# Kernel tuning notes

Hardware: AMD Instinct MI355X
Metric: run time of the kernel (lower is better)

Reference implementation:

```python
import jax, jax.numpy as jnp
import numpy as np

N, C, T, V = 16, 64, 512, 25
R, O, S = 8, 64, 3  # rel_channels, out_channels, num_subset


def setup_inputs() -> dict:
    key = jax.random.key(0)
    ks = jax.random.split(key, 12)
    sc = 0.05
    return {
        "x": jax.random.normal(ks[0], (N, C, T, V), jnp.float32),
        "A": jax.random.normal(ks[1], (S, V, V), jnp.float32) * 0.1,
        "alpha": jax.random.normal(ks[2], (1,), jnp.float32) * 0.1,
        "w1": jax.random.normal(ks[3], (S, R, C), jnp.float32) * sc,
        "b1": jax.random.normal(ks[4], (S, R), jnp.float32) * sc,
        "w2": jax.random.normal(ks[5], (S, R, C), jnp.float32) * sc,
        "b2": jax.random.normal(ks[6], (S, R), jnp.float32) * sc,
        "w3": jax.random.normal(ks[7], (S, O, C), jnp.float32) * sc,
        "b3": jax.random.normal(ks[8], (S, O), jnp.float32) * sc,
        "w4": jax.random.normal(ks[9], (S, O, R), jnp.float32) * sc,
        "b4": jax.random.normal(ks[10], (S, O), jnp.float32) * sc,
        "sparse": 0,
    }


def _mask(w, thr):
    # SparseConv2d: magnitude-threshold the 1x1 conv weights at runtime.
    return jnp.where(jnp.abs(w) > thr, w, jnp.zeros_like(w))


def reference(x, A, alpha, w1, b1, w2, b2, w3, b3, w4, b4, sparse):
    thr = jnp.float32(sparse)

    def conv1x1(w, b, inp):  # w [o,c], b [o], inp [n,c,t,v] -> [n,o,t,v]
        return jnp.einsum('oc,nctv->notv', _mask(w, thr), inp) + b[None, :, None, None]

    y = None
    for i in range(A.shape[0]):
        x1 = conv1x1(w1[i], b1[i], x).mean(-2)          # [n,r,v]
        x2 = conv1x1(w2[i], b2[i], x).mean(-2)          # [n,r,v]
        x3 = conv1x1(w3[i], b3[i], x)                   # [n,o,t,v]
        att = jnp.tanh(x1[..., :, None] - x2[..., None, :])  # [n,r,v,v]
        a = jnp.einsum('or,nruv->nouv', _mask(w4[i], thr), att) + b4[i][None, :, None, None]
        a = a * alpha + A[i][None, None]                # [n,o,v,v]
        z = jnp.einsum('ncuv,nctu->nctv', a, x3)        # node aggregation
        y = z if y is None else y + z
    # in_channels == out_channels -> residual is identity
    return jax.nn.relu(y + x)
```

## Files before the change

kernel.cpp:

```cpp
#include <hip/hip_runtime.h>
#include <cmath>

typedef __bf16 bf16x4v __attribute__((ext_vector_type(4)));
typedef __bf16 bf16x8 __attribute__((ext_vector_type(8)));
typedef float f32x4 __attribute__((ext_vector_type(4)));

namespace {
constexpr int kN = 16, kC = 64, kT = 512, kV = 25, kS = 3, kO = 64;
constexpr int kTV = kT * kV;
constexpr size_t WS_AFRAG = 102400;
constexpr size_t WS_W3F = WS_AFRAG + (size_t)48 * 131072;
constexpr size_t WS_XBF = WS_W3F + 3 * 8192;
}

__device__ __forceinline__ int swzB16(int c, int t, int ubyte) {
  return (c << 10) + (((t << 6) + ubyte) ^ ((((c ^ t) & 7)) << 4));
}

__global__ __launch_bounds__(256) void k1_cvt(const float* __restrict__ x,
                                              __bf16* __restrict__ xbf,
                                              float* __restrict__ xm) {
  const int bid = blockIdx.x;
  __shared__ float part[250][4];
  const int tid = threadIdx.x;
  const float4* xg4 = (const float4*)(x + (size_t)bid * kTV);
  bf16x4v* xb4 = (bf16x4v*)(xbf + (size_t)bid * kTV);
  if (tid < 250) {
    float a0 = 0.f, a1 = 0.f, a2 = 0.f, a3 = 0.f;
    for (int j = tid; j < 3200; j += 250) {
      float4 v = xg4[j];
      a0 += v.x; a1 += v.y; a2 += v.z; a3 += v.w;
      bf16x4v o;
      o[0] = (__bf16)v.x; o[1] = (__bf16)v.y;
      o[2] = (__bf16)v.z; o[3] = (__bf16)v.w;
      xb4[j] = o;
    }
    part[tid][0] = a0; part[tid][1] = a1; part[tid][2] = a2; part[tid][3] = a3;
  }
  __syncthreads();
  if (tid < 25) {
    float s = 0.f;
#pragma unroll
    for (int r = 0; r < 4; ++r) {
      int q = ((tid - r + 25) % 25) * 19 % 25;
#pragma unroll
      for (int p = 0; p < 10; ++p) s += part[q + 25 * p][r];
    }
    xm[bid * 25 + tid] = s * (1.f / 512.f);
  }
}

__global__ __launch_bounds__(256) void k2_attn(
    const float* __restrict__ xm, const float* __restrict__ Ag,
    const float* __restrict__ alpha, const float* __restrict__ w1,
    const float* __restrict__ b1, const float* __restrict__ w2,
    const float* __restrict__ b2, const float* __restrict__ w3,
    const float* __restrict__ w4, const float* __restrict__ b4,
    const int* __restrict__ sparse, unsigned char* __restrict__ ws) {
  const float thr = (float)sparse[0];
  const int b = blockIdx.x;
  const int s = b >> 6, n = (b >> 2) & 15, q = b & 3;
  __shared__ float xm_l[1600];
  __shared__ float x1_l[200], x2_l[200];
  __shared__ float att_l[8 * 625];
  __shared__ float attsum_l[200];
  __shared__ float ag_l[625];
  __shared__ float acs_l[25];
  __shared__ float w4_l[512];
  const int tid = threadIdx.x;
  for (int i = tid; i < 1600; i += 256) xm_l[i] = xm[n * 1600 + i];
  for (int i = tid; i < 512; i += 256) {
    float w = w4[s * 512 + i];
    w4_l[i] = (fabsf(w) > thr) ? w : 0.f;
  }
  for (int i = tid; i < 625; i += 256) ag_l[i] = Ag[s * 625 + i];
  __syncthreads();
  for (int i = tid; i < 400; i += 256) {
    int which = i / 200, idx = i % 200, r = idx / 25, u = idx % 25;
    const float* wrow = (which == 0 ? w1 : w2) + (s * 8 + r) * 64;
    float acc = 0.f;
    for (int cc = 0; cc < 64; ++cc) {
      float w = wrow[cc];
      w = (fabsf(w) > thr) ? w : 0.f;
      acc += w * xm_l[cc * 25 + u];
    }
    acc += (which == 0 ? b1 : b2)[s * 8 + r];
    if (which == 0) x1_l[idx] = acc;
    else x2_l[idx] = acc;
  }
  __syncthreads();
  for (int i = tid; i < 8 * 625; i += 256) {
    int r = i / 625, uv = i % 625, u = uv / 25, v = uv % 25;
    att_l[i] = tanhf(x1_l[r * 25 + u] - x2_l[r * 25 + v]);
  }
  __syncthreads();
  if (tid < 200) {
    int r = tid / 25, v = tid % 25;
    float sum = 0.f;
    for (int u = 0; u < 25; ++u) sum += att_l[r * 625 + u * 25 + v];
    attsum_l[tid] = sum;
  } else if (tid < 225) {
    int v = tid - 200;
    float sum = 0.f;
    for (int u = 0; u < 25; ++u) sum += ag_l[u * 25 + v];
    acs_l[v] = sum;
  }
  __syncthreads();
  const float al = alpha[0];
  unsigned char* afrag = ws + WS_AFRAG + (size_t)(s * 16 + n) * 131072;
  for (int slot = q * 2048 + tid; slot < (q + 1) * 2048; slot += 256) {
    int c = slot >> 7, vt = (slot >> 6) & 1, l = slot & 63;
    int v = vt * 16 + (l & 15), g = l >> 4;
    bf16x8 out;
    if (v < 25) {
      float b4v = b4[s * 64 + c];
#pragma unroll
      for (int j = 0; j < 8; ++j) {
        int u = g * 8 + j;
        float val = 0.f;
        if (u < 25) {
          float acc = 0.f;
#pragma unroll
          for (int r = 0; r < 8; ++r) acc += w4_l[c * 8 + r] * att_l[r * 625 + u * 25 + v];
          val = al * (acc + b4v) + ag_l[u * 25 + v];
        } else if (u == 25) {
          float acc = 0.f;
#pragma unroll
          for (int r = 0; r < 8; ++r) acc += w4_l[c * 8 + r] * attsum_l[r * 25 + v];
          val = al * acc + 25.f * al * b4v + acs_l[v];
        }
        out[j] = (__bf16)val;
      }
    } else {
#pragma unroll
      for (int j = 0; j < 8; ++j) out[j] = (__bf16)0.f;
    }
    *(bf16x8*)(afrag + (size_t)slot * 16) = out;
  }
  if (n == 0 && tid < 128) {
    unsigned char* w3f = ws + WS_W3F + (size_t)s * 8192;
    int slot = q * 128 + tid;
    int ot = slot >> 7, ks = (slot >> 6) & 1, l = slot & 63;
    int o = ot * 16 + (l & 15), g = l >> 4;
    bf16x8 out;
#pragma unroll
    for (int j = 0; j < 8; ++j) {
      int cp = ks * 32 + g * 8 + j;
      float w = w3[(s * 64 + o) * 64 + cp];
      out[j] = (__bf16)((fabsf(w) > thr) ? w : 0.f);
    }
    *(bf16x8*)(w3f + slot * 16) = out;
  }
}

__global__ __launch_bounds__(512) void k3_main(const __bf16* __restrict__ xbf,
                                               const float* __restrict__ b3,
                                               const unsigned char* __restrict__ ws,
                                               float* __restrict__ y) {
  const int n = blockIdx.x;
  const int tb = blockIdx.y;
  extern __shared__ __align__(16) unsigned char smem[];
  const int tid = threadIdx.x;
  const int w = tid >> 6, l = tid & 63, g = l >> 4, l15 = l & 15;

  for (int idx = tid; idx < 3072; idx += 512) {
    int pair = idx / 3, k = idx % 3;
    int c = pair >> 4, t = pair & 15;
    *(unsigned int*)(smem + swzB16(c, t, 52 + 4 * k)) = 0u;
  }

  bf16x8 xa[4][2];
#pragma unroll
  for (int cti = 0; cti < 4; ++cti)
#pragma unroll
    for (int kf = 0; kf < 2; ++kf)
#pragma unroll
      for (int j = 0; j < 8; ++j) xa[cti][kf][j] = (__bf16)0.f;
  {
    const __bf16* xbp = xbf + (size_t)n * kC * kTV;
#pragma unroll
    for (int cti = 0; cti < 4; ++cti) {
      int tt = tb * 16 + 2 * w + (cti >> 1);
      int u = (cti & 1) * 16 + l15;
      if (u < 25) {
#pragma unroll
        for (int kf = 0; kf < 2; ++kf)
#pragma unroll
          for (int j = 0; j < 8; ++j) {
            int cp = kf * 32 + g * 8 + j;
            xa[cti][kf][j] = xbp[(size_t)cp * kTV + tt * 25 + u];
          }
      }
    }
  }

  const unsigned char* afrag = ws + WS_AFRAG;
  const unsigned char* w3f = ws + WS_W3F;

  f32x4 zacc[8][2];
#pragma unroll
  for (int cc = 0; cc < 8; ++cc)
#pragma unroll
    for (int vt = 0; vt < 2; ++vt) {
      f32x4 zz = {0.f, 0.f, 0.f, 0.f};
      zacc[cc][vt] = zz;
    }

  for (int s = 0; s < kS; ++s) {
    bf16x8 B2[8][2];
    const unsigned char* af = afrag + (size_t)(s * 16 + n) * 131072;
#pragma unroll
    for (int cc = 0; cc < 8; ++cc) {
      int c = w * 8 + cc;
#pragma unroll
      for (int vt = 0; vt < 2; ++vt)
        B2[cc][vt] = *(const bf16x8*)(af + ((c * 2 + vt) * 64 + l) * 16);
    }
    ((f32x4*)(smem + 65536))[tid] =
        ((const f32x4*)(w3f + (size_t)s * 8192))[tid];
    __syncthreads();

    const unsigned char* w3l = smem + 65536;
#pragma unroll
    for (int ot = 0; ot < 4; ++ot) {
      bf16x8 wk0 = *(const bf16x8*)(w3l + ((ot * 2 + 0) * 64 + l) * 16);
      bf16x8 wk1 = *(const bf16x8*)(w3l + ((ot * 2 + 1) * 64 + l) * 16);
      int c = ot * 16 + l15;
#pragma unroll
      for (int cti = 0; cti < 4; ++cti) {
        f32x4 d = {0.f, 0.f, 0.f, 0.f};
        d = __builtin_amdgcn_mfma_f32_16x16x32_bf16(xa[cti][0], wk0, d, 0, 0, 0);
        d = __builtin_amdgcn_mfma_f32_16x16x32_bf16(xa[cti][1], wk1, d, 0, 0, 0);
        int tt = 2 * w + (cti >> 1);
        if (!(cti & 1)) {
          bf16x4v pk;
          pk[0] = (__bf16)d[0]; pk[1] = (__bf16)d[1];
          pk[2] = (__bf16)d[2]; pk[3] = (__bf16)d[3];
          *(bf16x4v*)(smem + swzB16(c, tt, g * 8)) = pk;
        } else if (g < 2) {
          bf16x4v pk;
          pk[0] = (__bf16)d[0]; pk[1] = (__bf16)d[1];
          pk[2] = (__bf16)d[2]; pk[3] = (__bf16)d[3];
          *(bf16x4v*)(smem + swzB16(c, tt, 32 + g * 8)) = pk;
        } else if (g == 2) {
          *(__bf16*)(smem + swzB16(c, tt, 48)) = (__bf16)d[0];
        }
      }
    }
    for (int i = tid; i < 1024; i += 512) {
      int c = i >> 4, t = i & 15;
      *(__bf16*)(smem + swzB16(c, t, 50)) = (__bf16)b3[s * 64 + c];
    }
    __syncthreads();
#pragma unroll
    for (int cc = 0; cc < 8; ++cc) {
      int c = w * 8 + cc;
      bf16x8 a2 = *(const bf16x8*)(smem + swzB16(c, l15, g * 16));
      zacc[cc][0] = __builtin_amdgcn_mfma_f32_16x16x32_bf16(a2, B2[cc][0], zacc[cc][0], 0, 0, 0);
      zacc[cc][1] = __builtin_amdgcn_mfma_f32_16x16x32_bf16(a2, B2[cc][1], zacc[cc][1], 0, 0, 0);
    }
  }
  __syncthreads();
  float* zs = (float*)smem;
  const __bf16* xbp = xbf + (size_t)n * kC * kTV;
  float4* yg4 = (float4*)(y + (size_t)n * kC * kTV);
#pragma unroll
  for (int h = 0; h < 2; ++h) {
    if ((w >> 2) == h) {
      int c0l = (w & 3) * 8;
#pragma unroll
      for (int cc = 0; cc < 8; ++cc)
#pragma unroll
        for (int vt = 0; vt < 2; ++vt) {
          int v = vt * 16 + l15;
          if (v < 25) {
#pragma unroll
            for (int jj = 0; jj < 4; ++jj)
              zs[(c0l + cc) * 400 + (g * 4 + jj) * 25 + v] = zacc[cc][vt][jj];
          }
        }
    }
    __syncthreads();
    for (int i4 = tid; i4 < 3200; i4 += 512) {
      int cl = i4 / 100, r4 = i4 % 100, c = h * 32 + cl;
      bf16x4v xv = *(const bf16x4v*)(xbp + (size_t)c * kTV + tb * 400 + r4 * 4);
      f32x4 zv = *(const f32x4*)(zs + cl * 400 + r4 * 4);
      float4 o;
      o.x = fmaxf(zv[0] + (float)xv[0], 0.f);
      o.y = fmaxf(zv[1] + (float)xv[1], 0.f);
      o.z = fmaxf(zv[2] + (float)xv[2], 0.f);
      o.w = fmaxf(zv[3] + (float)xv[3], 0.f);
      yg4[c * 3200 + tb * 100 + r4] = o;
    }
    __syncthreads();
  }
}

extern "C" void kernel_launch(void* const* d_in, const int* in_sizes, int n_in,
                              void* d_out, int out_size, void* d_ws, size_t ws_size,
                              hipStream_t stream) {
  const float* x = (const float*)d_in[0];
  const float* Ag = (const float*)d_in[1];
  const float* alpha = (const float*)d_in[2];
  const float* w1 = (const float*)d_in[3];
  const float* b1 = (const float*)d_in[4];
  const float* w2 = (const float*)d_in[5];
  const float* b2 = (const float*)d_in[6];
  const float* w3 = (const float*)d_in[7];
  const float* b3 = (const float*)d_in[8];
  const float* w4 = (const float*)d_in[9];
  const float* b4 = (const float*)d_in[10];
  const int* sparse = (const int*)d_in[11];

  unsigned char* ws = (unsigned char*)d_ws;
  float* xm = (float*)ws;
  __bf16* xbf = (__bf16*)(ws + WS_XBF);
  float* y = (float*)d_out;

  hipFuncSetAttribute((const void*)k3_main,
                      hipFuncAttributeMaxDynamicSharedMemorySize, 73728);

  k1_cvt<<<kN * kC, 256, 0, stream>>>(x, xbf, xm);
  k2_attn<<<kS * kN * 4, 256, 0, stream>>>(xm, Ag, alpha, w1, b1, w2, b2, w3, w4,
                                           b4, sparse, ws);
  dim3 g3(kN, kT / 16);
  k3_main<<<g3, 512, 73728, stream>>>(xbf, b3, ws, y);
}
```

Before: 74.49 us.

## Fuse three kernels into one cooperative kernel with grid-wide syncs

```diff
diff --git a/kernel.cpp b/kernel.cpp
--- a/kernel.cpp
+++ b/kernel.cpp
@@ -1,5 +1,8 @@
 #include <hip/hip_runtime.h>
+#include <hip/hip_cooperative_groups.h>
 #include <cmath>
+
+namespace cg = cooperative_groups;
 
 typedef __bf16 bf16x4v __attribute__((ext_vector_type(4)));
 typedef __bf16 bf16x8 __attribute__((ext_vector_type(8)));
@@ -17,167 +20,180 @@
   return (c << 10) + (((t << 6) + ubyte) ^ ((((c ^ t) & 7)) << 4));
 }
 
-__global__ __launch_bounds__(256) void k1_cvt(const float* __restrict__ x,
-                                              __bf16* __restrict__ xbf,
-                                              float* __restrict__ xm) {
-  const int bid = blockIdx.x;
-  __shared__ float part[250][4];
-  const int tid = threadIdx.x;
-  const float4* xg4 = (const float4*)(x + (size_t)bid * kTV);
-  bf16x4v* xb4 = (bf16x4v*)(xbf + (size_t)bid * kTV);
-  if (tid < 250) {
-    float a0 = 0.f, a1 = 0.f, a2 = 0.f, a3 = 0.f;
-    for (int j = tid; j < 3200; j += 250) {
-      float4 v = xg4[j];
-      a0 += v.x; a1 += v.y; a2 += v.z; a3 += v.w;
-      bf16x4v o;
-      o[0] = (__bf16)v.x; o[1] = (__bf16)v.y;
-      o[2] = (__bf16)v.z; o[3] = (__bf16)v.w;
-      xb4[j] = o;
-    }
-    part[tid][0] = a0; part[tid][1] = a1; part[tid][2] = a2; part[tid][3] = a3;
-  }
-  __syncthreads();
-  if (tid < 25) {
-    float s = 0.f;
-#pragma unroll
-    for (int r = 0; r < 4; ++r) {
-      int q = ((tid - r + 25) % 25) * 19 % 25;
-#pragma unroll
-      for (int p = 0; p < 10; ++p) s += part[q + 25 * p][r];
-    }
-    xm[bid * 25 + tid] = s * (1.f / 512.f);
-  }
-}
-
-__global__ __launch_bounds__(256) void k2_attn(
-    const float* __restrict__ xm, const float* __restrict__ Ag,
+__global__ __launch_bounds__(512) void k_fused(
+    const float* __restrict__ x, const float* __restrict__ Ag,
     const float* __restrict__ alpha, const float* __restrict__ w1,
     const float* __restrict__ b1, const float* __restrict__ w2,
     const float* __restrict__ b2, const float* __restrict__ w3,
-    const float* __restrict__ w4, const float* __restrict__ b4,
-    const int* __restrict__ sparse, unsigned char* __restrict__ ws) {
-  const float thr = (float)sparse[0];
+    const float* __restrict__ b3, const float* __restrict__ w4,
+    const float* __restrict__ b4, const int* __restrict__ sparse,
+    unsigned char* __restrict__ ws, float* __restrict__ y) {
+  cg::grid_group grid = cg::this_grid();
+  extern __shared__ __align__(16) unsigned char smem[];
   const int b = blockIdx.x;
-  const int s = b >> 6, n = (b >> 2) & 15, q = b & 3;
-  __shared__ float xm_l[1600];
-  __shared__ float x1_l[200], x2_l[200];
-  __shared__ float att_l[8 * 625];
-  __shared__ float attsum_l[200];
-  __shared__ float ag_l[625];
-  __shared__ float acs_l[25];
-  __shared__ float w4_l[512];
   const int tid = threadIdx.x;
-  for (int i = tid; i < 1600; i += 256) xm_l[i] = xm[n * 1600 + i];
-  for (int i = tid; i < 512; i += 256) {
-    float w = w4[s * 512 + i];
-    w4_l[i] = (fabsf(w) > thr) ? w : 0.f;
+
+  float* xm = (float*)ws;
+  __bf16* xbf = (__bf16*)(ws + WS_XBF);
+
+  {
+    const int half = tid >> 8;
+    const int lt = tid & 255;
+    float* part = (float*)smem + half * 1000;
+#pragma unroll
+    for (int pr = 0; pr < 2; ++pr) {
+      const int colid = b * 4 + pr * 2 + half;
+      const float4* xg4 = (const float4*)(x + (size_t)colid * kTV);
+      bf16x4v* xb4 = (bf16x4v*)(xbf + (size_t)colid * kTV);
+      if (lt < 250) {
+        float a0 = 0.f, a1 = 0.f, a2 = 0.f, a3 = 0.f;
+        for (int j = lt; j < 3200; j += 250) {
+          float4 v = xg4[j];
+          a0 += v.x; a1 += v.y; a2 += v.z; a3 += v.w;
+          bf16x4v o;
+          o[0] = (__bf16)v.x; o[1] = (__bf16)v.y;
+          o[2] = (__bf16)v.z; o[3] = (__bf16)v.w;
+          xb4[j] = o;
+        }
+        part[lt * 4 + 0] = a0; part[lt * 4 + 1] = a1;
+        part[lt * 4 + 2] = a2; part[lt * 4 + 3] = a3;
+      }
+      __syncthreads();
+      if (lt < 25) {
+        float s = 0.f;
+#pragma unroll
+        for (int r = 0; r < 4; ++r) {
+          int q = ((lt - r + 25) % 25) * 19 % 25;
+#pragma unroll
+          for (int p = 0; p < 10; ++p) s += part[(q + 25 * p) * 4 + r];
+        }
+        xm[colid * 25 + lt] = s * (1.f / 512.f);
+      }
+      __syncthreads();
+    }
   }
-  for (int i = tid; i < 625; i += 256) ag_l[i] = Ag[s * 625 + i];
-  __syncthreads();
-  for (int i = tid; i < 400; i += 256) {
-    int which = i / 200, idx = i % 200, r = idx / 25, u = idx % 25;
-    const float* wrow = (which == 0 ? w1 : w2) + (s * 8 + r) * 64;
-    float acc = 0.f;
-    for (int cc = 0; cc < 64; ++cc) {
-      float w = wrow[cc];
-      w = (fabsf(w) > thr) ? w : 0.f;
-      acc += w * xm_l[cc * 25 + u];
-    }
-    acc += (which == 0 ? b1 : b2)[s * 8 + r];
-    if (which == 0) x1_l[idx] = acc;
-    else x2_l[idx] = acc;
+  grid.sync();
+
+  if (b < 192) {
+    const float thr = (float)sparse[0];
+    const int s = b >> 6, n = (b >> 2) & 15, q = b & 3;
+    float* xm_l = (float*)smem;
+    float* x1_l = xm_l + 1600;
+    float* x2_l = x1_l + 200;
+    float* att_l = x2_l + 200;
+    float* attsum_l = att_l + 5000;
+    float* ag_l = attsum_l + 200;
+    float* acs_l = ag_l + 625;
+    float* w4_l = acs_l + 25;
+    for (int i = tid; i < 1600; i += 512) xm_l[i] = xm[n * 1600 + i];
+    for (int i = tid; i < 512; i += 512) {
+      float w = w4[s * 512 + i];
+      w4_l[i] = (fabsf(w) > thr) ? w : 0.f;
+    }
+    for (int i = tid; i < 625; i += 512) ag_l[i] = Ag[s * 625 + i];
+    __syncthreads();
+    for (int i = tid; i < 400; i += 512) {
+      int which = i / 200, idx = i % 200, r = idx / 25, u = idx % 25;
+      const float* wrow = (which == 0 ? w1 : w2) + (s * 8 + r) * 64;
+      float acc = 0.f;
+      for (int cc = 0; cc < 64; ++cc) {
+        float w = wrow[cc];
+        w = (fabsf(w) > thr) ? w : 0.f;
+        acc += w * xm_l[cc * 25 + u];
+      }
+      acc += (which == 0 ? b1 : b2)[s * 8 + r];
+      if (which == 0) x1_l[idx] = acc;
+      else x2_l[idx] = acc;
+    }
+    __syncthreads();
+    for (int i = tid; i < 8 * 625; i += 512) {
+      int r = i / 625, uv = i % 625, u = uv / 25, v = uv % 25;
+      att_l[i] = tanhf(x1_l[r * 25 + u] - x2_l[r * 25 + v]);
+    }
+    __syncthreads();
+    if (tid < 200) {
+      int r = tid / 25, v = tid % 25;
+      float sum = 0.f;
+      for (int u = 0; u < 25; ++u) sum += att_l[r * 625 + u * 25 + v];
+      attsum_l[tid] = sum;
+    } else if (tid < 225) {
+      int v = tid - 200;
+      float sum = 0.f;
+      for (int u = 0; u < 25; ++u) sum += ag_l[u * 25 + v];
+      acs_l[v] = sum;
+    }
+    __syncthreads();
+    const float al = alpha[0];
+    unsigned char* afrag = ws + WS_AFRAG + (size_t)(s * 16 + n) * 131072;
+    for (int slot = q * 2048 + tid; slot < (q + 1) * 2048; slot += 512) {
+      int c = slot >> 7, vt = (slot >> 6) & 1, l = slot & 63;
+      int v = vt * 16 + (l & 15), g = l >> 4;
+      bf16x8 out;
+      if (v < 25) {
+        float b4v = b4[s * 64 + c];
+#pragma unroll
+        for (int j = 0; j < 8; ++j) {
+          int u = g * 8 + j;
+          float val = 0.f;
+          if (u < 25) {
+            float acc = 0.f;
+#pragma unroll
+            for (int r = 0; r < 8; ++r)
+              acc += w4_l[c * 8 + r] * att_l[r * 625 + u * 25 + v];
+            val = al * (acc + b4v) + ag_l[u * 25 + v];
+          } else if (u == 25) {
+            float acc = 0.f;
+#pragma unroll
+            for (int r = 0; r < 8; ++r)
+              acc += w4_l[c * 8 + r] * attsum_l[r * 25 + v];
+            val = al * acc + 25.f * al * b4v + acs_l[v];
+          }
+          out[j] = (__bf16)val;
+        }
+      } else {
+#pragma unroll
+        for (int j = 0; j < 8; ++j) out[j] = (__bf16)0.f;
+      }
+      *(bf16x8*)(afrag + (size_t)slot * 16) = out;
+    }
+    if (n == 0 && tid < 128) {
+      unsigned char* w3f = ws + WS_W3F + (size_t)s * 8192;
+      int slot = q * 128 + tid;
+      int ot = slot >> 7, ks = (slot >> 6) & 1, l = slot & 63;
+      int o = ot * 16 + (l & 15), g = l >> 4;
+      bf16x8 out;
+#pragma unroll
+      for (int j = 0; j < 8; ++j) {
+        int cp = ks * 32 + g * 8 + j;
+        float w = w3[(s * 64 + o) * 64 + cp];
+        out[j] = (__bf16)((fabsf(w) > thr) ? w : 0.f);
+      }
+      *(bf16x8*)(w3f + slot * 16) = out;
+    }
   }
-  __syncthreads();
-  for (int i = tid; i < 8 * 625; i += 256) {
-    int r = i / 625, uv = i % 625, u = uv / 25, v = uv % 25;
-    att_l[i] = tanhf(x1_l[r * 25 + u] - x2_l[r * 25 + v]);
-  }
-  __syncthreads();
-  if (tid < 200) {
-    int r = tid / 25, v = tid % 25;
-    float sum = 0.f;
-    for (int u = 0; u < 25; ++u) sum += att_l[r * 625 + u * 25 + v];
-    attsum_l[tid] = sum;
-  } else if (tid < 225) {
-    int v = tid - 200;
-    float sum = 0.f;
-    for (int u = 0; u < 25; ++u) sum += ag_l[u * 25 + v];
-    acs_l[v] = sum;
-  }
-  __syncthreads();
-  const float al = alpha[0];
-  unsigned char* afrag = ws + WS_AFRAG + (size_t)(s * 16 + n) * 131072;
-  for (int slot = q * 2048 + tid; slot < (q + 1) * 2048; slot += 256) {
-    int c = slot >> 7, vt = (slot >> 6) & 1, l = slot & 63;
-    int v = vt * 16 + (l & 15), g = l >> 4;
-    bf16x8 out;
-    if (v < 25) {
-      float b4v = b4[s * 64 + c];
-#pragma unroll
-      for (int j = 0; j < 8; ++j) {
-        int u = g * 8 + j;
-        float val = 0.f;
-        if (u < 25) {
-          float acc = 0.f;
-#pragma unroll
-          for (int r = 0; r < 8; ++r) acc += w4_l[c * 8 + r] * att_l[r * 625 + u * 25 + v];
-          val = al * (acc + b4v) + ag_l[u * 25 + v];
-        } else if (u == 25) {
-          float acc = 0.f;
-#pragma unroll
-          for (int r = 0; r < 8; ++r) acc += w4_l[c * 8 + r] * attsum_l[r * 25 + v];
-          val = al * acc + 25.f * al * b4v + acs_l[v];
-        }
-        out[j] = (__bf16)val;
-      }
-    } else {
-#pragma unroll
-      for (int j = 0; j < 8; ++j) out[j] = (__bf16)0.f;
-    }
-    *(bf16x8*)(afrag + (size_t)slot * 16) = out;
-  }
-  if (n == 0 && tid < 128) {
-    unsigned char* w3f = ws + WS_W3F + (size_t)s * 8192;
-    int slot = q * 128 + tid;
-    int ot = slot >> 7, ks = (slot >> 6) & 1, l = slot & 63;
-    int o = ot * 16 + (l & 15), g = l >> 4;
-    bf16x8 out;
-#pragma unroll
-    for (int j = 0; j < 8; ++j) {
-      int cp = ks * 32 + g * 8 + j;
-      float w = w3[(s * 64 + o) * 64 + cp];
-      out[j] = (__bf16)((fabsf(w) > thr) ? w : 0.f);
-    }
-    *(bf16x8*)(w3f + slot * 16) = out;
-  }
-}
-
-__global__ __launch_bounds__(512) void k3_main(const __bf16* __restrict__ xbf,
-                                               const float* __restrict__ b3,
-                                               const unsigned char* __restrict__ ws,
-                                               float* __restrict__ y) {
-  const int n = blockIdx.x;
-  const int tb = blockIdx.y;
-  extern __shared__ __align__(16) unsigned char smem[];
-  const int tid = threadIdx.x;
+  grid.sync();
+
   const int w = tid >> 6, l = tid & 63, g = l >> 4, l15 = l & 15;
-
-  for (int idx = tid; idx < 3072; idx += 512) {
-    int pair = idx / 3, k = idx % 3;
-    int c = pair >> 4, t = pair & 15;
-    *(unsigned int*)(smem + swzB16(c, t, 52 + 4 * k)) = 0u;
-  }
-
-  bf16x8 xa[4][2];
-#pragma unroll
-  for (int cti = 0; cti < 4; ++cti)
-#pragma unroll
-    for (int kf = 0; kf < 2; ++kf)
-#pragma unroll
-      for (int j = 0; j < 8; ++j) xa[cti][kf][j] = (__bf16)0.f;
-  {
-    const __bf16* xbp = xbf + (size_t)n * kC * kTV;
+  const int n = b >> 4;
+  const unsigned char* afrag = ws + WS_AFRAG;
+  const unsigned char* w3f = ws + WS_W3F;
+  const __bf16* xbp = xbf + (size_t)n * kC * kTV;
+
+  for (int unit = 0; unit < 2; ++unit) {
+    const int tb = ((b & 15) << 1) | unit;
+    __syncthreads();
+    for (int idx = tid; idx < 3072; idx += 512) {
+      int pair = idx / 3, k = idx % 3;
+      int c = pair >> 4, t = pair & 15;
+      *(unsigned int*)(smem + swzB16(c, t, 52 + 4 * k)) = 0u;
+    }
+    bf16x8 xa[4][2];
+#pragma unroll
+    for (int cti = 0; cti < 4; ++cti)
+#pragma unroll
+      for (int kf = 0; kf < 2; ++kf)
+#pragma unroll
+        for (int j = 0; j < 8; ++j) xa[cti][kf][j] = (__bf16)0.f;
 #pragma unroll
     for (int cti = 0; cti < 4; ++cti) {
       int tt = tb * 16 + 2 * w + (cti >> 1);
@@ -192,107 +208,103 @@
           }
       }
     }
-  }
-
-  const unsigned char* afrag = ws + WS_AFRAG;
-  const unsigned char* w3f = ws + WS_W3F;
-
-  f32x4 zacc[8][2];
-#pragma unroll
-  for (int cc = 0; cc < 8; ++cc)
-#pragma unroll
-    for (int vt = 0; vt < 2; ++vt) {
-      f32x4 zz = {0.f, 0.f, 0.f, 0.f};
-      zacc[cc][vt] = zz;
-    }
-
-  for (int s = 0; s < kS; ++s) {
-    bf16x8 B2[8][2];
-    const unsigned char* af = afrag + (size_t)(s * 16 + n) * 131072;
-#pragma unroll
-    for (int cc = 0; cc < 8; ++cc) {
-      int c = w * 8 + cc;
-#pragma unroll
-      for (int vt = 0; vt < 2; ++vt)
-        B2[cc][vt] = *(const bf16x8*)(af + ((c * 2 + vt) * 64 + l) * 16);
-    }
-    ((f32x4*)(smem + 65536))[tid] =
-        ((const f32x4*)(w3f + (size_t)s * 8192))[tid];
-    __syncthreads();
-
-    const unsigned char* w3l = smem + 65536;
-#pragma unroll
-    for (int ot = 0; ot < 4; ++ot) {
-      bf16x8 wk0 = *(const bf16x8*)(w3l + ((ot * 2 + 0) * 64 + l) * 16);
-      bf16x8 wk1 = *(const bf16x8*)(w3l + ((ot * 2 + 1) * 64 + l) * 16);
-      int c = ot * 16 + l15;
-#pragma unroll
-      for (int cti = 0; cti < 4; ++cti) {
-        f32x4 d = {0.f, 0.f, 0.f, 0.f};
-        d = __builtin_amdgcn_mfma_f32_16x16x32_bf16(xa[cti][0], wk0, d, 0, 0, 0);
-        d = __builtin_amdgcn_mfma_f32_16x16x32_bf16(xa[cti][1], wk1, d, 0, 0, 0);
-        int tt = 2 * w + (cti >> 1);
-        if (!(cti & 1)) {
-          bf16x4v pk;
-          pk[0] = (__bf16)d[0]; pk[1] = (__bf16)d[1];
-          pk[2] = (__bf16)d[2]; pk[3] = (__bf16)d[3];
-          *(bf16x4v*)(smem + swzB16(c, tt, g * 8)) = pk;
-        } else if (g < 2) {
-          bf16x4v pk;
-          pk[0] = (__bf16)d[0]; pk[1] = (__bf16)d[1];
-          pk[2] = (__bf16)d[2]; pk[3] = (__bf16)d[3];
-          *(bf16x4v*)(smem + swzB16(c, tt, 32 + g * 8)) = pk;
-        } else if (g == 2) {
-          *(__bf16*)(smem + swzB16(c, tt, 48)) = (__bf16)d[0];
-        }
-      }
-    }
-    for (int i = tid; i < 1024; i += 512) {
-      int c = i >> 4, t = i & 15;
-      *(__bf16*)(smem + swzB16(c, t, 50)) = (__bf16)b3[s * 64 + c];
-    }
-    __syncthreads();
-#pragma unroll
-    for (int cc = 0; cc < 8; ++cc) {
-      int c = w * 8 + cc;
-      bf16x8 a2 = *(const bf16x8*)(smem + swzB16(c, l15, g * 16));
-      zacc[cc][0] = __builtin_amdgcn_mfma_f32_16x16x32_bf16(a2, B2[cc][0], zacc[cc][0], 0, 0, 0);
-      zacc[cc][1] = __builtin_amdgcn_mfma_f32_16x16x32_bf16(a2, B2[cc][1], zacc[cc][1], 0, 0, 0);
-    }
-  }
-  __syncthreads();
-  float* zs = (float*)smem;
-  const __bf16* xbp = xbf + (size_t)n * kC * kTV;
-  float4* yg4 = (float4*)(y + (size_t)n * kC * kTV);
-#pragma unroll
-  for (int h = 0; h < 2; ++h) {
-    if ((w >> 2) == h) {
-      int c0l = (w & 3) * 8;
-#pragma unroll
-      for (int cc = 0; cc < 8; ++cc)
-#pragma unroll
-        for (int vt = 0; vt < 2; ++vt) {
-          int v = vt * 16 + l15;
-          if (v < 25) {
-#pragma unroll
-            for (int jj = 0; jj < 4; ++jj)
-              zs[(c0l + cc) * 400 + (g * 4 + jj) * 25 + v] = zacc[cc][vt][jj];
+
+    f32x4 zacc[8][2];
+#pragma unroll
+    for (int cc = 0; cc < 8; ++cc)
+#pragma unroll
+      for (int vt = 0; vt < 2; ++vt) {
+        f32x4 zz = {0.f, 0.f, 0.f, 0.f};
+        zacc[cc][vt] = zz;
+      }
+
+    for (int s = 0; s < kS; ++s) {
+      bf16x8 B2[8][2];
+      const unsigned char* af = afrag + (size_t)(s * 16 + n) * 131072;
+#pragma unroll
+      for (int cc = 0; cc < 8; ++cc) {
+        int c = w * 8 + cc;
+#pragma unroll
+        for (int vt = 0; vt < 2; ++vt)
+          B2[cc][vt] = *(const bf16x8*)(af + ((c * 2 + vt) * 64 + l) * 16);
+      }
+      ((f32x4*)(smem + 65536))[tid] =
+          ((const f32x4*)(w3f + (size_t)s * 8192))[tid];
+      __syncthreads();
+
+      const unsigned char* w3l = smem + 65536;
+#pragma unroll
+      for (int ot = 0; ot < 4; ++ot) {
+        bf16x8 wk0 = *(const bf16x8*)(w3l + ((ot * 2 + 0) * 64 + l) * 16);
+        bf16x8 wk1 = *(const bf16x8*)(w3l + ((ot * 2 + 1) * 64 + l) * 16);
+        int c = ot * 16 + l15;
+#pragma unroll
+        for (int cti = 0; cti < 4; ++cti) {
+          f32x4 d = {0.f, 0.f, 0.f, 0.f};
+          d = __builtin_amdgcn_mfma_f32_16x16x32_bf16(xa[cti][0], wk0, d, 0, 0, 0);
+          d = __builtin_amdgcn_mfma_f32_16x16x32_bf16(xa[cti][1], wk1, d, 0, 0, 0);
+          int tt = 2 * w + (cti >> 1);
+          if (!(cti & 1)) {
+            bf16x4v pk;
+            pk[0] = (__bf16)d[0]; pk[1] = (__bf16)d[1];
+            pk[2] = (__bf16)d[2]; pk[3] = (__bf16)d[3];
+            *(bf16x4v*)(smem + swzB16(c, tt, g * 8)) = pk;
+          } else if (g < 2) {
+            bf16x4v pk;
+            pk[0] = (__bf16)d[0]; pk[1] = (__bf16)d[1];
+            pk[2] = (__bf16)d[2]; pk[3] = (__bf16)d[3];
+            *(bf16x4v*)(smem + swzB16(c, tt, 32 + g * 8)) = pk;
+          } else if (g == 2) {
+            *(__bf16*)(smem + swzB16(c, tt, 48)) = (__bf16)d[0];
           }
         }
-    }
-    __syncthreads();
-    for (int i4 = tid; i4 < 3200; i4 += 512) {
-      int cl = i4 / 100, r4 = i4 % 100, c = h * 32 + cl;
-      bf16x4v xv = *(const bf16x4v*)(xbp + (size_t)c * kTV + tb * 400 + r4 * 4);
-      f32x4 zv = *(const f32x4*)(zs + cl * 400 + r4 * 4);
-      float4 o;
-      o.x = fmaxf(zv[0] + (float)xv[0], 0.f);
-      o.y = fmaxf(zv[1] + (float)xv[1], 0.f);
-      o.z = fmaxf(zv[2] + (float)xv[2], 0.f);
-      o.w = fmaxf(zv[3] + (float)xv[3], 0.f);
-      yg4[c * 3200 + tb * 100 + r4] = o;
-    }
-    __syncthreads();
+      }
+      for (int i = tid; i < 1024; i += 512) {
+        int c = i >> 4, t = i & 15;
+        *(__bf16*)(smem + swzB16(c, t, 50)) = (__bf16)b3[s * 64 + c];
+      }
+      __syncthreads();
+#pragma unroll
+      for (int cc = 0; cc < 8; ++cc) {
+        int c = w * 8 + cc;
+        bf16x8 a2 = *(const bf16x8*)(smem + swzB16(c, l15, g * 16));
+        zacc[cc][0] = __builtin_amdgcn_mfma_f32_16x16x32_bf16(a2, B2[cc][0], zacc[cc][0], 0, 0, 0);
+        zacc[cc][1] = __builtin_amdgcn_mfma_f32_16x16x32_bf16(a2, B2[cc][1], zacc[cc][1], 0, 0, 0);
+      }
+    }
+    __syncthreads();
+    float* zs = (float*)smem;
+    float4* yg4 = (float4*)(y + (size_t)n * kC * kTV);
+#pragma unroll
+    for (int h = 0; h < 2; ++h) {
+      if ((w >> 2) == h) {
+        int c0l = (w & 3) * 8;
+#pragma unroll
+        for (int cc = 0; cc < 8; ++cc)
+#pragma unroll
+          for (int vt = 0; vt < 2; ++vt) {
+            int v = vt * 16 + l15;
+            if (v < 25) {
+#pragma unroll
+              for (int jj = 0; jj < 4; ++jj)
+                zs[(c0l + cc) * 400 + (g * 4 + jj) * 25 + v] = zacc[cc][vt][jj];
+            }
+          }
+      }
+      __syncthreads();
+      for (int i4 = tid; i4 < 3200; i4 += 512) {
+        int cl = i4 / 100, r4 = i4 % 100, c = h * 32 + cl;
+        bf16x4v xv = *(const bf16x4v*)(xbp + (size_t)c * kTV + tb * 400 + r4 * 4);
+        f32x4 zv = *(const f32x4*)(zs + cl * 400 + r4 * 4);
+        float4 o;
+        o.x = fmaxf(zv[0] + (float)xv[0], 0.f);
+        o.y = fmaxf(zv[1] + (float)xv[1], 0.f);
+        o.z = fmaxf(zv[2] + (float)xv[2], 0.f);
+        o.w = fmaxf(zv[3] + (float)xv[3], 0.f);
+        yg4[c * 3200 + tb * 100 + r4] = o;
+      }
+      __syncthreads();
+    }
   }
 }
 
@@ -313,16 +325,15 @@
   const int* sparse = (const int*)d_in[11];
 
   unsigned char* ws = (unsigned char*)d_ws;
-  float* xm = (float*)ws;
-  __bf16* xbf = (__bf16*)(ws + WS_XBF);
   float* y = (float*)d_out;
 
-  hipFuncSetAttribute((const void*)k3_main,
+  hipFuncSetAttribute((const void*)k_fused,
                       hipFuncAttributeMaxDynamicSharedMemorySize, 73728);
 
-  k1_cvt<<<kN * kC, 256, 0, stream>>>(x, xbf, xm);
-  k2_attn<<<kS * kN * 4, 256, 0, stream>>>(xm, Ag, alpha, w1, b1, w2, b2, w3, w4,
-                                           b4, sparse, ws);
-  dim3 g3(kN, kT / 16);
-  k3_main<<<g3, 512, 73728, stream>>>(xbf, b3, ws, y);
+  void* args[] = {(void*)&x,  (void*)&Ag, (void*)&alpha, (void*)&w1,
+                  (void*)&b1, (void*)&w2, (void*)&b2,    (void*)&w3,
+                  (void*)&b3, (void*)&w4, (void*)&b4,    (void*)&sparse,
+                  (void*)&ws, (void*)&y};
+  hipLaunchCooperativeKernel((const void*)k_fused, dim3(256), dim3(512), args,
+                             73728, stream);
 }
```

Result: slower. 135.1 us (+81.4%).
